# Kernel optimization log

Hardware: AMD Instinct MI355X
Metric: run time of the kernel (lower is better)

The kernel has to match this reference:

```python
import jax, jax.numpy as jnp
import numpy as np
import math

N, T, D, H = 8, 1024, 768, 12

def setup_inputs() -> dict:
    key = jax.random.key(0)
    ks = jax.random.split(key, 5)
    s = 1.0 / math.sqrt(D)
    return {
        "x": jax.random.normal(ks[0], (N, T, D), dtype=jnp.float32),
        "Wq": jax.random.normal(ks[1], (D, D), dtype=jnp.float32) * s,
        "Wk": jax.random.normal(ks[2], (D, D), dtype=jnp.float32) * s,
        "Wv": jax.random.normal(ks[3], (D, D), dtype=jnp.float32) * s,
        "Wo": jax.random.normal(ks[4], (D, D), dtype=jnp.float32) * s,
        "bo": jnp.zeros((D,), dtype=jnp.float32),
    }

def reference(x, Wq, Wk, Wv, Wo, bo):
    n, t, d = x.shape
    h = H
    dh = d // h  # 64
    # nn.Linear: y = x @ W.T
    q = (x @ Wq.T).reshape(n, t, h, dh).transpose(0, 2, 1, 3)  # [n,h,t,dh]
    k = (x @ Wk.T).reshape(n, t, h, dh).transpose(0, 2, 1, 3)
    v = (x @ Wv.T).reshape(n, t, h, dh).transpose(0, 2, 1, 3)
    scores = jnp.einsum('nhqd,nhkd->nhqk', q, k) / math.sqrt(dh)  # [n,h,t,t]
    causal = jnp.tril(jnp.ones((t, t), dtype=bool))
    scores = jnp.where(causal, scores, -jnp.inf)
    attn = jax.nn.softmax(scores, axis=-1)
    out = jnp.einsum('nhqk,nhkd->nhqd', attn, v)  # [n,h,t,dh]
    out = out.transpose(0, 2, 1, 3).reshape(n, t, d)
    return out @ Wo.T + bo
```

## Files before the change

kernel.cpp:

```cpp
#include <hip/hip_runtime.h>

typedef __attribute__((ext_vector_type(8))) short short8;
typedef __attribute__((ext_vector_type(4))) float f32x4;
typedef __attribute__((ext_vector_type(4))) short short4v;
typedef __attribute__((ext_vector_type(4))) unsigned short ushort4v;

#define DEV static __device__ __forceinline__

DEV unsigned short f2bf(float f) {
  unsigned int u = __builtin_bit_cast(unsigned int, f);
  u += 0x7fffu + ((u >> 16) & 1u);
  return (unsigned short)(u >> 16);
}

DEV unsigned int pack2bf(float a, float b) {
  return (unsigned int)f2bf(a) | ((unsigned int)f2bf(b) << 16);
}

DEV void gload16(const void* g, void* l) {
  __builtin_amdgcn_global_load_lds(
      (const __attribute__((address_space(1))) unsigned int*)g,
      (__attribute__((address_space(3))) unsigned int*)l, 16, 0, 0);
}

__global__ __launch_bounds__(256) void cvt_bf16(const float* __restrict__ in,
                                                unsigned short* __restrict__ out,
                                                int nvec4) {
  int i = blockIdx.x * 256 + threadIdx.x;
  if (i >= nvec4) return;
  float4 v = ((const float4*)in)[i];
  ushort4v o = {f2bf(v.x), f2bf(v.y), f2bf(v.z), f2bf(v.w)};
  *(ushort4v*)(out + (size_t)i * 4) = o;
}

template <int MODE>
__global__ __launch_bounds__(256) void gemm_bt(const short* __restrict__ A,
                                               const short* __restrict__ B,
                                               void* __restrict__ Cout,
                                               const float* __restrict__ bias) {
  __shared__ short As[128 * 32];
  __shared__ short Bs[128 * 32];
  const int tid = threadIdx.x;
  const int lane = tid & 63;
  const int wave = tid >> 6;
  const int row0 = blockIdx.x * 128;
  const int col0 = blockIdx.y * 128;
  const int wr = (wave >> 1) * 64;
  const int wc = (wave & 1) * 64;

  f32x4 acc[4][4] = {};

  const short* aG = A + (size_t)(row0 + wave * 16 + (lane >> 2)) * 768 + (lane & 3) * 8;
  const short* bG = B + (size_t)(col0 + wave * 16 + (lane >> 2)) * 768 + (lane & 3) * 8;
  char* aL = (char*)As + wave * 1024;
  char* bL = (char*)Bs + wave * 1024;

  const int cl = lane & 15;
  const int g8 = (lane >> 4) * 8;

  for (int kk = 0; kk < 768; kk += 32) {
    gload16(aG + kk, aL);
    gload16(aG + 64 * 768 + kk, aL + 4096);
    gload16(bG + kk, bL);
    gload16(bG + 64 * 768 + kk, bL + 4096);
    __syncthreads();
    short8 af[4], bfr[4];
#pragma unroll
    for (int m = 0; m < 4; m++) af[m] = *(const short8*)&As[(wr + m * 16 + cl) * 32 + g8];
#pragma unroll
    for (int n = 0; n < 4; n++) bfr[n] = *(const short8*)&Bs[(wc + n * 16 + cl) * 32 + g8];
#pragma unroll
    for (int m = 0; m < 4; m++)
#pragma unroll
      for (int n = 0; n < 4; n++)
        acc[m][n] = __builtin_amdgcn_mfma_f32_16x16x32_bf16(af[m], bfr[n], acc[m][n], 0, 0, 0);
    __syncthreads();
  }

  const int r4 = (lane >> 4) * 4;
#pragma unroll
  for (int m = 0; m < 4; m++) {
#pragma unroll
    for (int n = 0; n < 4; n++) {
#pragma unroll
      for (int r = 0; r < 4; r++) {
        const int row = row0 + wr + m * 16 + r4 + r;
        const int col = col0 + wc + n * 16 + cl;
        const float v = acc[m][n][r];
        if (MODE == 0) {
          ((unsigned short*)Cout)[(size_t)((((row >> 10) * 12 + (col >> 6)) << 16) +
                                           ((row & 1023) << 6) + (col & 63))] = f2bf(v);
        } else if (MODE == 1) {
          ((unsigned short*)Cout)[(size_t)((((row >> 10) * 12 + (col >> 6)) << 16) +
                                           ((col & 63) << 10) + (row & 1023))] = f2bf(v);
        } else {
          ((float*)Cout)[(size_t)row * 768 + col] = v + bias[col];
        }
      }
    }
  }
}

__global__ __launch_bounds__(256) void attn_fwd(const short* __restrict__ Qh,
                                                const short* __restrict__ Kh,
                                                const short* __restrict__ Vt,
                                                short* __restrict__ Obuf) {
  __shared__ short Ks[32 * 72];
  __shared__ short Vs[64 * 40];
  __shared__ unsigned int Ps[4][16 * 36];

  const int tid = threadIdx.x;
  const int lane = tid & 63;
  const int w = tid >> 6;
  const int qb = blockIdx.x;
  const int nh = blockIdx.y;
  const int nIdx = nh / 12;
  const int hIdx = nh % 12;
  const int hb = nh << 16;
  const int qr0 = qb * 64 + w * 16;
  const int qloc = lane & 15;
  const int g = lane >> 4;
  const int qg = qr0 + qloc;

  short8 qf[2];
  qf[0] = *(const short8*)&Qh[hb + qg * 64 + g * 8];
  qf[1] = *(const short8*)&Qh[hb + qg * 64 + 32 + g * 8];

  float m_run = -INFINITY, l_run = 0.f;
  f32x4 o[4] = {};

  const int kv_end = qb * 64 + 64;
  const int qmax = qr0 + 15;
  const int kRow = tid >> 3, kColB = (tid & 7) * 8;
  const int vRow = tid >> 2, vColB = (tid & 3) * 8;

  for (int kv0 = 0; kv0 < kv_end; kv0 += 32) {
    *(short8*)&Ks[kRow * 72 + kColB] = *(const short8*)&Kh[hb + (kv0 + kRow) * 64 + kColB];
    *(short8*)&Vs[vRow * 40 + vColB] = *(const short8*)&Vt[hb + vRow * 1024 + kv0 + vColB];
    __syncthreads();
    if (kv0 <= qmax) {
      f32x4 s[2] = {};
#pragma unroll
      for (int c = 0; c < 2; c++) {
        short8 a0 = *(const short8*)&Ks[qloc * 72 + c * 32 + g * 8];
        short8 a1 = *(const short8*)&Ks[(16 + qloc) * 72 + c * 32 + g * 8];
        s[0] = __builtin_amdgcn_mfma_f32_16x16x32_bf16(a0, qf[c], s[0], 0, 0, 0);
        s[1] = __builtin_amdgcn_mfma_f32_16x16x32_bf16(a1, qf[c], s[1], 0, 0, 0);
      }
      float pv[2][4];
      float pm = -INFINITY;
#pragma unroll
      for (int kt = 0; kt < 2; kt++)
#pragma unroll
        for (int r = 0; r < 4; r++) {
          const int kg = kv0 + kt * 16 + g * 4 + r;
          float sv = s[kt][r] * 0.125f;
          sv = (kg <= qg) ? sv : -INFINITY;
          pv[kt][r] = sv;
          pm = fmaxf(pm, sv);
        }
      pm = fmaxf(pm, __shfl_xor(pm, 16));
      pm = fmaxf(pm, __shfl_xor(pm, 32));
      const float mnew = fmaxf(m_run, pm);
      const float corr = __expf(m_run - mnew);
      float lsum = 0.f;
#pragma unroll
      for (int kt = 0; kt < 2; kt++)
#pragma unroll
        for (int r = 0; r < 4; r++) {
          float p = __expf(pv[kt][r] - mnew);
          pv[kt][r] = p;
          lsum += p;
        }
      lsum += __shfl_xor(lsum, 16);
      lsum += __shfl_xor(lsum, 32);
      l_run = l_run * corr + lsum;
      m_run = mnew;
#pragma unroll
      for (int dt = 0; dt < 4; dt++) o[dt] *= corr;
      unsigned int* pr = &Ps[w][qloc * 36];
#pragma unroll
      for (int kt = 0; kt < 2; kt++) {
        pr[kt * 8 + g * 2] = pack2bf(pv[kt][0], pv[kt][1]);
        pr[kt * 8 + g * 2 + 1] = pack2bf(pv[kt][2], pv[kt][3]);
      }
      __asm__ volatile("" ::: "memory");
      short8 pf = *(const short8*)((const short*)&Ps[w][0] + qloc * 72 + g * 8);
#pragma unroll
      for (int dt = 0; dt < 4; dt++) {
        short8 vf = *(const short8*)&Vs[(dt * 16 + qloc) * 40 + g * 8];
        o[dt] = __builtin_amdgcn_mfma_f32_16x16x32_bf16(vf, pf, o[dt], 0, 0, 0);
      }
    }
    __syncthreads();
  }

  const float inv = 1.f / l_run;
  const int outRow = nIdx * 1024 + qr0 + qloc;
  short* op = Obuf + (size_t)outRow * 768 + hIdx * 64;
#pragma unroll
  for (int dt = 0; dt < 4; dt++) {
    short4v ov;
#pragma unroll
    for (int r = 0; r < 4; r++) ov[r] = (short)f2bf(o[dt][r] * inv);
    *(short4v*)(op + dt * 16 + g * 4) = ov;
  }
}

extern "C" void kernel_launch(void* const* d_in, const int* in_sizes, int n_in,
                              void* d_out, int out_size, void* d_ws, size_t ws_size,
                              hipStream_t stream) {
  (void)in_sizes; (void)n_in; (void)out_size; (void)ws_size;
  const float* x  = (const float*)d_in[0];
  const float* Wq = (const float*)d_in[1];
  const float* Wk = (const float*)d_in[2];
  const float* Wv = (const float*)d_in[3];
  const float* Wo = (const float*)d_in[4];
  const float* bo = (const float*)d_in[5];

  char* ws = (char*)d_ws;
  short* xb  = (short*)(ws);
  short* wqb = (short*)(ws + 12582912);
  short* wkb = (short*)(ws + 12582912 + 1179648);
  short* wvb = (short*)(ws + 12582912 + 2 * 1179648);
  short* wob = (short*)(ws + 12582912 + 3 * 1179648);
  short* Qh  = (short*)(ws + 17301504);
  short* Kh  = (short*)(ws + 17301504 + 12582912);
  short* Vt  = (short*)(ws + 17301504 + 2 * 12582912);
  short* Ob  = (short*)(ws + 17301504 + 3 * 12582912);

  cvt_bf16<<<6144, 256, 0, stream>>>(x, (unsigned short*)xb, 1572864);
  cvt_bf16<<<576, 256, 0, stream>>>(Wq, (unsigned short*)wqb, 147456);
  cvt_bf16<<<576, 256, 0, stream>>>(Wk, (unsigned short*)wkb, 147456);
  cvt_bf16<<<576, 256, 0, stream>>>(Wv, (unsigned short*)wvb, 147456);
  cvt_bf16<<<576, 256, 0, stream>>>(Wo, (unsigned short*)wob, 147456);

  dim3 gg(64, 6);
  gemm_bt<0><<<gg, 256, 0, stream>>>(xb, wqb, Qh, nullptr);
  gemm_bt<0><<<gg, 256, 0, stream>>>(xb, wkb, Kh, nullptr);
  gemm_bt<1><<<gg, 256, 0, stream>>>(xb, wvb, Vt, nullptr);

  attn_fwd<<<dim3(16, 96), 256, 0, stream>>>(Qh, Kh, Vt, Ob);

  gemm_bt<2><<<gg, 256, 0, stream>>>(Ob, wob, d_out, bo);
}
```

Measured before the change: 246.4 us.

## Fuse weight casts and QKV GEMMs, pair causal query blocks in attention

Merges the four weight conversion launches into one kernel and the three Q/K/V projection GEMMs into a single launch with a 64x18 grid, cutting launch overhead and letting all 1152 tiles run at once. The attention kernel now processes two query blocks per workgroup, one from the front and its mirror (15-qb) from the back, so each workgroup does the same amount of causal work. The grid halves to 8x96, which reduces the number of concurrent workgroups in exchange for better load balance.

Measured after the change: 225.9 us. 1.09x faster.

```diff
diff --git a/kernel.cpp b/kernel.cpp
--- a/kernel.cpp
+++ b/kernel.cpp
@@ -33,11 +33,92 @@
   *(ushort4v*)(out + (size_t)i * 4) = o;
 }
 
-template <int MODE>
-__global__ __launch_bounds__(256) void gemm_bt(const short* __restrict__ A,
-                                               const short* __restrict__ B,
-                                               void* __restrict__ Cout,
-                                               const float* __restrict__ bias) {
+__global__ __launch_bounds__(256) void cvt_w4(const float* __restrict__ w0,
+                                              const float* __restrict__ w1,
+                                              const float* __restrict__ w2,
+                                              const float* __restrict__ w3,
+                                              unsigned short* __restrict__ out) {
+  int i = blockIdx.x * 256 + threadIdx.x;
+  int wsel = i / 147456;
+  int j = i - wsel * 147456;
+  const float* src = wsel == 0 ? w0 : wsel == 1 ? w1 : wsel == 2 ? w2 : w3;
+  float4 v = ((const float4*)src)[j];
+  ushort4v o = {f2bf(v.x), f2bf(v.y), f2bf(v.z), f2bf(v.w)};
+  *(ushort4v*)(out + (size_t)i * 4) = o;
+}
+
+__global__ __launch_bounds__(256) void gemm_qkv(const short* __restrict__ A,
+                                                const short* __restrict__ B0,
+                                                unsigned short* __restrict__ QK,
+                                                unsigned short* __restrict__ Vt) {
+  __shared__ short As[128 * 32];
+  __shared__ short Bs[128 * 32];
+  const int tid = threadIdx.x;
+  const int lane = tid & 63;
+  const int wave = tid >> 6;
+  const int row0 = blockIdx.x * 128;
+  const int wsel = blockIdx.y / 6;
+  const int col0 = (blockIdx.y % 6) * 128;
+  const short* B = B0 + (size_t)wsel * 589824;
+  const int wr = (wave >> 1) * 64;
+  const int wc = (wave & 1) * 64;
+
+  f32x4 acc[4][4] = {};
+
+  const short* aG = A + (size_t)(row0 + wave * 16 + (lane >> 2)) * 768 + (lane & 3) * 8;
+  const short* bG = B + (size_t)(col0 + wave * 16 + (lane >> 2)) * 768 + (lane & 3) * 8;
+  char* aL = (char*)As + wave * 1024;
+  char* bL = (char*)Bs + wave * 1024;
+
+  const int cl = lane & 15;
+  const int g8 = (lane >> 4) * 8;
+
+  for (int kk = 0; kk < 768; kk += 32) {
+    gload16(aG + kk, aL);
+    gload16(aG + 64 * 768 + kk, aL + 4096);
+    gload16(bG + kk, bL);
+    gload16(bG + 64 * 768 + kk, bL + 4096);
+    __syncthreads();
+    short8 af[4], bfr[4];
+#pragma unroll
+    for (int m = 0; m < 4; m++) af[m] = *(const short8*)&As[(wr + m * 16 + cl) * 32 + g8];
+#pragma unroll
+    for (int n = 0; n < 4; n++) bfr[n] = *(const short8*)&Bs[(wc + n * 16 + cl) * 32 + g8];
+#pragma unroll
+    for (int m = 0; m < 4; m++)
+#pragma unroll
+      for (int n = 0; n < 4; n++)
+        acc[m][n] = __builtin_amdgcn_mfma_f32_16x16x32_bf16(af[m], bfr[n], acc[m][n], 0, 0, 0);
+    __syncthreads();
+  }
+
+  const int r4 = (lane >> 4) * 4;
+  unsigned short* Qout = QK + (size_t)wsel * 6291456;
+#pragma unroll
+  for (int m = 0; m < 4; m++) {
+#pragma unroll
+    for (int n = 0; n < 4; n++) {
+#pragma unroll
+      for (int r = 0; r < 4; r++) {
+        const int row = row0 + wr + m * 16 + r4 + r;
+        const int col = col0 + wc + n * 16 + cl;
+        const unsigned short v = f2bf(acc[m][n][r]);
+        if (wsel < 2) {
+          Qout[(size_t)((((row >> 10) * 12 + (col >> 6)) << 16) +
+                        ((row & 1023) << 6) + (col & 63))] = v;
+        } else {
+          Vt[(size_t)((((row >> 10) * 12 + (col >> 6)) << 16) +
+                      ((col & 63) << 10) + (row & 1023))] = v;
+        }
+      }
+    }
+  }
+}
+
+__global__ __launch_bounds__(256) void gemm_out(const short* __restrict__ A,
+                                                const short* __restrict__ B,
+                                                float* __restrict__ Cout,
+                                                const float* __restrict__ bias) {
   __shared__ short As[128 * 32];
   __shared__ short Bs[128 * 32];
   const int tid = threadIdx.x;
@@ -86,16 +167,7 @@
       for (int r = 0; r < 4; r++) {
         const int row = row0 + wr + m * 16 + r4 + r;
         const int col = col0 + wc + n * 16 + cl;
-        const float v = acc[m][n][r];
-        if (MODE == 0) {
-          ((unsigned short*)Cout)[(size_t)((((row >> 10) * 12 + (col >> 6)) << 16) +
-                                           ((row & 1023) << 6) + (col & 63))] = f2bf(v);
-        } else if (MODE == 1) {
-          ((unsigned short*)Cout)[(size_t)((((row >> 10) * 12 + (col >> 6)) << 16) +
-                                           ((col & 63) << 10) + (row & 1023))] = f2bf(v);
-        } else {
-          ((float*)Cout)[(size_t)row * 768 + col] = v + bias[col];
-        }
+        Cout[(size_t)row * 768 + col] = acc[m][n][r] + bias[col];
       }
     }
   }
@@ -112,98 +184,100 @@
   const int tid = threadIdx.x;
   const int lane = tid & 63;
   const int w = tid >> 6;
-  const int qb = blockIdx.x;
   const int nh = blockIdx.y;
   const int nIdx = nh / 12;
   const int hIdx = nh % 12;
   const int hb = nh << 16;
-  const int qr0 = qb * 64 + w * 16;
   const int qloc = lane & 15;
   const int g = lane >> 4;
-  const int qg = qr0 + qloc;
-
-  short8 qf[2];
-  qf[0] = *(const short8*)&Qh[hb + qg * 64 + g * 8];
-  qf[1] = *(const short8*)&Qh[hb + qg * 64 + 32 + g * 8];
-
-  float m_run = -INFINITY, l_run = 0.f;
-  f32x4 o[4] = {};
-
-  const int kv_end = qb * 64 + 64;
-  const int qmax = qr0 + 15;
   const int kRow = tid >> 3, kColB = (tid & 7) * 8;
   const int vRow = tid >> 2, vColB = (tid & 3) * 8;
 
-  for (int kv0 = 0; kv0 < kv_end; kv0 += 32) {
-    *(short8*)&Ks[kRow * 72 + kColB] = *(const short8*)&Kh[hb + (kv0 + kRow) * 64 + kColB];
-    *(short8*)&Vs[vRow * 40 + vColB] = *(const short8*)&Vt[hb + vRow * 1024 + kv0 + vColB];
-    __syncthreads();
-    if (kv0 <= qmax) {
-      f32x4 s[2] = {};
-#pragma unroll
-      for (int c = 0; c < 2; c++) {
-        short8 a0 = *(const short8*)&Ks[qloc * 72 + c * 32 + g * 8];
-        short8 a1 = *(const short8*)&Ks[(16 + qloc) * 72 + c * 32 + g * 8];
-        s[0] = __builtin_amdgcn_mfma_f32_16x16x32_bf16(a0, qf[c], s[0], 0, 0, 0);
-        s[1] = __builtin_amdgcn_mfma_f32_16x16x32_bf16(a1, qf[c], s[1], 0, 0, 0);
+  for (int rep = 0; rep < 2; rep++) {
+    const int qb = rep ? (15 - blockIdx.x) : blockIdx.x;
+    const int qr0 = qb * 64 + w * 16;
+    const int qg = qr0 + qloc;
+    const int qmax = qr0 + 15;
+    const int kv_end = qb * 64 + 64;
+
+    short8 qf[2];
+    qf[0] = *(const short8*)&Qh[hb + qg * 64 + g * 8];
+    qf[1] = *(const short8*)&Qh[hb + qg * 64 + 32 + g * 8];
+
+    float m_run = -INFINITY, l_run = 0.f;
+    f32x4 o[4] = {};
+
+    for (int kv0 = 0; kv0 < kv_end; kv0 += 32) {
+      *(short8*)&Ks[kRow * 72 + kColB] = *(const short8*)&Kh[hb + (kv0 + kRow) * 64 + kColB];
+      *(short8*)&Vs[vRow * 40 + vColB] = *(const short8*)&Vt[hb + vRow * 1024 + kv0 + vColB];
+      __syncthreads();
+      if (kv0 <= qmax) {
+        f32x4 s[2] = {};
+#pragma unroll
+        for (int c = 0; c < 2; c++) {
+          short8 a0 = *(const short8*)&Ks[qloc * 72 + c * 32 + g * 8];
+          short8 a1 = *(const short8*)&Ks[(16 + qloc) * 72 + c * 32 + g * 8];
+          s[0] = __builtin_amdgcn_mfma_f32_16x16x32_bf16(a0, qf[c], s[0], 0, 0, 0);
+          s[1] = __builtin_amdgcn_mfma_f32_16x16x32_bf16(a1, qf[c], s[1], 0, 0, 0);
+        }
+        float pv[2][4];
+        float pm = -INFINITY;
+#pragma unroll
+        for (int kt = 0; kt < 2; kt++)
+#pragma unroll
+          for (int r = 0; r < 4; r++) {
+            const int kg = kv0 + kt * 16 + g * 4 + r;
+            float sv = s[kt][r] * 0.125f;
+            sv = (kg <= qg) ? sv : -INFINITY;
+            pv[kt][r] = sv;
+            pm = fmaxf(pm, sv);
+          }
+        pm = fmaxf(pm, __shfl_xor(pm, 16));
+        pm = fmaxf(pm, __shfl_xor(pm, 32));
+        const float mnew = fmaxf(m_run, pm);
+        const float corr = __expf(m_run - mnew);
+        float lsum = 0.f;
+#pragma unroll
+        for (int kt = 0; kt < 2; kt++)
+#pragma unroll
+          for (int r = 0; r < 4; r++) {
+            float p = __expf(pv[kt][r] - mnew);
+            pv[kt][r] = p;
+            lsum += p;
+          }
+        lsum += __shfl_xor(lsum, 16);
+        lsum += __shfl_xor(lsum, 32);
+        l_run = l_run * corr + lsum;
+        m_run = mnew;
+#pragma unroll
+        for (int dt = 0; dt < 4; dt++) o[dt] *= corr;
+        unsigned int* pr = &Ps[w][qloc * 36];
+#pragma unroll
+        for (int kt = 0; kt < 2; kt++) {
+          pr[kt * 8 + g * 2] = pack2bf(pv[kt][0], pv[kt][1]);
+          pr[kt * 8 + g * 2 + 1] = pack2bf(pv[kt][2], pv[kt][3]);
+        }
+        __asm__ volatile("" ::: "memory");
+        short8 pf = *(const short8*)((const short*)&Ps[w][0] + qloc * 72 + g * 8);
+#pragma unroll
+        for (int dt = 0; dt < 4; dt++) {
+          short8 vf = *(const short8*)&Vs[(dt * 16 + qloc) * 40 + g * 8];
+          o[dt] = __builtin_amdgcn_mfma_f32_16x16x32_bf16(vf, pf, o[dt], 0, 0, 0);
+        }
       }
-      float pv[2][4];
-      float pm = -INFINITY;
-#pragma unroll
-      for (int kt = 0; kt < 2; kt++)
-#pragma unroll
-        for (int r = 0; r < 4; r++) {
-          const int kg = kv0 + kt * 16 + g * 4 + r;
-          float sv = s[kt][r] * 0.125f;
-          sv = (kg <= qg) ? sv : -INFINITY;
-          pv[kt][r] = sv;
-          pm = fmaxf(pm, sv);
-        }
-      pm = fmaxf(pm, __shfl_xor(pm, 16));
-      pm = fmaxf(pm, __shfl_xor(pm, 32));
-      const float mnew = fmaxf(m_run, pm);
-      const float corr = __expf(m_run - mnew);
-      float lsum = 0.f;
-#pragma unroll
-      for (int kt = 0; kt < 2; kt++)
-#pragma unroll
-        for (int r = 0; r < 4; r++) {
-          float p = __expf(pv[kt][r] - mnew);
-          pv[kt][r] = p;
-          lsum += p;
-        }
-      lsum += __shfl_xor(lsum, 16);
-      lsum += __shfl_xor(lsum, 32);
-      l_run = l_run * corr + lsum;
-      m_run = mnew;
-#pragma unroll
-      for (int dt = 0; dt < 4; dt++) o[dt] *= corr;
-      unsigned int* pr = &Ps[w][qloc * 36];
-#pragma unroll
-      for (int kt = 0; kt < 2; kt++) {
-        pr[kt * 8 + g * 2] = pack2bf(pv[kt][0], pv[kt][1]);
-        pr[kt * 8 + g * 2 + 1] = pack2bf(pv[kt][2], pv[kt][3]);
-      }
-      __asm__ volatile("" ::: "memory");
-      short8 pf = *(const short8*)((const short*)&Ps[w][0] + qloc * 72 + g * 8);
-#pragma unroll
-      for (int dt = 0; dt < 4; dt++) {
-        short8 vf = *(const short8*)&Vs[(dt * 16 + qloc) * 40 + g * 8];
-        o[dt] = __builtin_amdgcn_mfma_f32_16x16x32_bf16(vf, pf, o[dt], 0, 0, 0);
-      }
+      __syncthreads();
     }
-    __syncthreads();
-  }
-
-  const float inv = 1.f / l_run;
-  const int outRow = nIdx * 1024 + qr0 + qloc;
-  short* op = Obuf + (size_t)outRow * 768 + hIdx * 64;
-#pragma unroll
-  for (int dt = 0; dt < 4; dt++) {
-    short4v ov;
-#pragma unroll
-    for (int r = 0; r < 4; r++) ov[r] = (short)f2bf(o[dt][r] * inv);
-    *(short4v*)(op + dt * 16 + g * 4) = ov;
+
+    const float inv = 1.f / l_run;
+    const int outRow = nIdx * 1024 + qr0 + qloc;
+    short* op = Obuf + (size_t)outRow * 768 + hIdx * 64;
+#pragma unroll
+    for (int dt = 0; dt < 4; dt++) {
+      short4v ov;
+#pragma unroll
+      for (int r = 0; r < 4; r++) ov[r] = (short)f2bf(o[dt][r] * inv);
+      *(short4v*)(op + dt * 16 + g * 4) = ov;
+    }
   }
 }
 
@@ -221,8 +295,6 @@
   char* ws = (char*)d_ws;
   short* xb  = (short*)(ws);
   short* wqb = (short*)(ws + 12582912);
-  short* wkb = (short*)(ws + 12582912 + 1179648);
-  short* wvb = (short*)(ws + 12582912 + 2 * 1179648);
   short* wob = (short*)(ws + 12582912 + 3 * 1179648);
   short* Qh  = (short*)(ws + 17301504);
   short* Kh  = (short*)(ws + 17301504 + 12582912);
@@ -230,17 +302,12 @@
   short* Ob  = (short*)(ws + 17301504 + 3 * 12582912);
 
   cvt_bf16<<<6144, 256, 0, stream>>>(x, (unsigned short*)xb, 1572864);
-  cvt_bf16<<<576, 256, 0, stream>>>(Wq, (unsigned short*)wqb, 147456);
-  cvt_bf16<<<576, 256, 0, stream>>>(Wk, (unsigned short*)wkb, 147456);
-  cvt_bf16<<<576, 256, 0, stream>>>(Wv, (unsigned short*)wvb, 147456);
-  cvt_bf16<<<576, 256, 0, stream>>>(Wo, (unsigned short*)wob, 147456);
-
-  dim3 gg(64, 6);
-  gemm_bt<0><<<gg, 256, 0, stream>>>(xb, wqb, Qh, nullptr);
-  gemm_bt<0><<<gg, 256, 0, stream>>>(xb, wkb, Kh, nullptr);
-  gemm_bt<1><<<gg, 256, 0, stream>>>(xb, wvb, Vt, nullptr);
-
-  attn_fwd<<<dim3(16, 96), 256, 0, stream>>>(Qh, Kh, Vt, Ob);
-
-  gemm_bt<2><<<gg, 256, 0, stream>>>(Ob, wob, d_out, bo);
-}
+  cvt_w4<<<2304, 256, 0, stream>>>(Wq, Wk, Wv, Wo, (unsigned short*)wqb);
+
+  gemm_qkv<<<dim3(64, 18), 256, 0, stream>>>(xb, wqb, (unsigned short*)Qh,
+                                             (unsigned short*)Vt);
+
+  attn_fwd<<<dim3(8, 96), 256, 0, stream>>>(Qh, Kh, Vt, Ob);
+
+  gemm_out<<<dim3(64, 6), 256, 0, stream>>>(Ob, wob, (float*)d_out, bo);
+}
```
